# Kernel tuning notes

Measured on AMD Instinct MI355X. Metric: run time of the kernel, lower is better.

The kernel has to match this reference:

```python
import jax, jax.numpy as jnp
import numpy as np
from math import factorial, pi

LMAX = 6      # max angular momentum
NMAX = 5      # max radial index
RC = 3.0      # PolyCut cutoff radius
UNIT = RC / 3.0

_one = np.ones((LMAX + 1, LMAX + 1), np.float32)
YR = jnp.asarray(2.0 * np.tril(_one) - np.eye(LMAX + 1, dtype=np.float32))
YI = jnp.asarray(2.0 * np.triu(_one, k=1))


def _nlm(l, m):
    return float(np.sqrt((2 * l + 1) / (4 * pi) * factorial(l - m) / factorial(l + m)))


def ylm_mat(v):
    """Solid harmonics r^l Y_lm for one point v=(x,y,z).
    Layout (as in AutoForce sph_repr): Re Y_l^m at [l, l-m]; Im Y_l^m at [l-m, l] for m>0,
    so YR (2*tril-eye) weights real parts (m=0 on the diagonal, weight 1) and
    YI (2*triu(1)) weights imaginary parts, reproducing the m-sum of the power spectrum."""
    x, y, z = v[0], v[1], v[2]
    r2 = x * x + y * y + z * z
    # (x + i y)^m by recursion
    A = [jnp.ones((), v.dtype)]
    B = [jnp.zeros((), v.dtype)]
    for m in range(1, LMAX + 1):
        A.append(x * A[m - 1] - y * B[m - 1])
        B.append(x * B[m - 1] + y * A[m - 1])
    # Pi_l^m(z, r^2): homogeneous associated-Legendre part of degree l-m
    Pi = {(0, 0): jnp.ones((), v.dtype)}
    for m in range(1, LMAX + 1):
        Pi[(m, m)] = (2 * m - 1) * Pi[(m - 1, m - 1)]  # (2m-1)!!
    for m in range(0, LMAX):
        Pi[(m + 1, m)] = (2 * m + 1) * z * Pi[(m, m)]
        for l in range(m + 2, LMAX + 1):
            Pi[(l, m)] = ((2 * l - 1) * z * Pi[(l - 1, m)]
                          - (l + m - 1) * r2 * Pi[(l - 2, m)]) / (l - m)
    Y = jnp.zeros((LMAX + 1, LMAX + 1), v.dtype)
    for l in range(LMAX + 1):
        for m in range(l + 1):
            cnl = _nlm(l, m)
            Y = Y.at[l, l - m].set(cnl * Pi[(l, m)] * A[m])
            if m > 0:
                Y = Y.at[l - m, l].set(cnl * Pi[(l, m)] * B[m])
    return Y


def radial(dist):
    # PolyCut: (1 - d/rc)^2 inside rc, and its derivative
    step = (dist < RC).astype(dist.dtype)
    t = 1.0 - dist / RC
    return step * t * t, -2.0 * step * t / RC


def setup_inputs() -> dict:
    key = jax.random.key(0)
    coo = jax.random.normal(key, (150000, 3), dtype=jnp.float32)
    return {"coo": coo}


def reference(coo):
    xyz = coo / UNIT                                   # (N, 3)
    d = jnp.sqrt(jnp.sum(xyz * xyz, axis=-1))          # (N,)
    n = 2.0 * jnp.arange(NMAX + 1, dtype=coo.dtype)    # even powers 0,2,...,2*nmax
    r, dr = radial(UNIT * d)
    dr = UNIT * dr
    f = r[None] * d[None] ** n[:, None]                # (nmax+1, N)
    Y = jnp.transpose(jax.vmap(ylm_mat)(xyz), (1, 2, 0))                   # (L+1, L+1, N)
    dY = jnp.transpose(jax.vmap(jax.jacfwd(ylm_mat))(xyz), (1, 2, 0, 3))   # (L+1, L+1, N, 3)
    c = jnp.einsum('nj,lmj->nlm', f, Y)                # (nmax+1, L+1, L+1)
    # p[i,k,l] = sum_m YR[l,m]*c[i,l,m]*c[k,l,m] + sum_m YI[m,l]*c[i,m,l]*c[k,m,l]
    p = (jnp.einsum('ilm,klm,lm->ikl', c, c, YR)
         + jnp.einsum('iml,kml,ml->ikl', c, c, YI))    # (nmax+1, nmax+1, L+1)
    # hand-derived gradient chain, as in the torch module
    df = dr[None] * d[None] ** n[:, None] + r[None] * n[:, None] * d[None] ** (n[:, None] - 1.0)
    dfv = df[..., None] * xyz / d[:, None]             # (nmax+1, N, 3)
    dc = (dfv[:, None, None] * Y[None, ..., None]
          + f[:, None, None, :, None] * dY[None])      # (nmax+1, L+1, L+1, N, 3)
    # dp without materializing dnnp: contract dc with (c*YR) / (c*YI) directly
    cYr = c * YR
    cYi = c * YI
    dp = (jnp.einsum('klm,ilmjx->ikljx', cYr, dc)
          + jnp.einsum('ilm,klmjx->ikljx', cYr, dc)
          + jnp.einsum('kml,imljx->ikljx', cYi, dc)
          + jnp.einsum('iml,kmljx->ikljx', cYi, dc))   # (nmax+1, nmax+1, L+1, N, 3)
    return p, dp / UNIT
```

## Files before the change

kernel.cpp:

```cpp
#include <hip/hip_runtime.h>


#define LMAXV 6
#define NSZ 6
#define RCV 3.0f

constexpr double csqrt_(double x) {
    double y = x > 1.0 ? x : 1.0;
    for (int i = 0; i < 100; ++i) y = 0.5 * (y + x / y);
    return y;
}
constexpr double factd_(int n) { double r = 1.0; for (int i = 2; i <= n; ++i) r *= i; return r; }
constexpr double PI_D = 3.14159265358979323846;
struct CnlT { float v[7][7]; };
constexpr CnlT make_cnl_() {
    CnlT t{};
    for (int l = 0; l <= 6; ++l)
        for (int m = 0; m <= 6; ++m)
            t.v[l][m] = (m <= l)
                ? (float)csqrt_((2.0 * l + 1.0) / (4.0 * PI_D) * factd_(l - m) / factd_(l + m))
                : 0.0f;
    return t;
}
__device__ constexpr CnlT CNL = make_cnl_();
__device__ constexpr float DFACT[7] = {1.f, 1.f, 3.f, 15.f, 105.f, 945.f, 10395.f};
struct IctT { float v[7][7]; };
constexpr IctT make_ict_() {
    IctT t{};
    for (int l = 0; l <= 6; ++l)
        for (int m = 0; m <= 6; ++m)
            t.v[l][m] = (l > m) ? (float)(1.0 / (double)(l - m)) : 1.0f;
    return t;
}
__device__ constexpr IctT ICT = make_ict_();

__global__ void k_zero(float* __restrict__ cws) {
    int t = blockIdx.x * blockDim.x + threadIdx.x;
    if (t < NSZ * 49) cws[t] = 0.0f;
}

__global__ __launch_bounds__(256) void k_creduce(const float* __restrict__ coo,
                                                 float* __restrict__ cws, int N) {
    const int i_rad = blockIdx.y;
    float acc[7][7];
#pragma unroll
    for (int a = 0; a < 7; ++a)
#pragma unroll
        for (int b = 0; b < 7; ++b) acc[a][b] = 0.0f;

    const int stride = gridDim.x * blockDim.x;
    for (int j = blockIdx.x * blockDim.x + threadIdx.x; j < N; j += stride) {
        float x = coo[3 * j + 0], y = coo[3 * j + 1], z = coo[3 * j + 2];
        float r2 = x * x + y * y + z * z;
        float dn = sqrtf(r2);
        float tt = 1.0f - dn * (1.0f / RCV);
        float r  = (dn < RCV) ? tt * tt : 0.0f;
        float fi = r;
        for (int q = 0; q < i_rad; ++q) fi *= r2;

        float Av[7], Bv[7];
        Av[0] = 1.0f; Bv[0] = 0.0f;
#pragma unroll
        for (int m = 1; m <= 6; ++m) {
            Av[m] = x * Av[m - 1] - y * Bv[m - 1];
            Bv[m] = x * Bv[m - 1] + y * Av[m - 1];
        }

        float P1[7], P2[7];
#pragma unroll
        for (int l = 0; l <= 6; ++l) {
            float PC[7];
#pragma unroll
            for (int mm = 0; mm <= l; ++mm) {
                float pv;
                if (mm == l)            pv = DFACT[l];
                else if (mm == l - 1)   pv = (float)(2 * l - 1) * z * P1[mm];
                else {
                    float a = (float)(2 * l - 1), b = (float)(l + mm - 1);
                    pv = (a * z * P1[mm] - b * r2 * P2[mm]) * (1.0f / (float)(l - mm));
                }
                PC[mm] = pv;
                float base = fi * CNL.v[l][mm] * pv;
                acc[l][l - mm] += base * Av[mm];
                if (mm >= 1) acc[l - mm][l] += base * Bv[mm];
            }
#pragma unroll
            for (int mm = 0; mm <= l; ++mm) { P2[mm] = P1[mm]; P1[mm] = PC[mm]; }
        }
    }

    __shared__ float sblk[49];
    if (threadIdx.x < 49) sblk[threadIdx.x] = 0.0f;
    __syncthreads();
    const int lane = threadIdx.x & 63;
#pragma unroll
    for (int a = 0; a < 7; ++a)
#pragma unroll
        for (int b = 0; b < 7; ++b) {
            float v = acc[a][b];
            v += __shfl_down(v, 32);
            v += __shfl_down(v, 16);
            v += __shfl_down(v, 8);
            v += __shfl_down(v, 4);
            v += __shfl_down(v, 2);
            v += __shfl_down(v, 1);
            if (lane == 0) atomicAdd(&sblk[a * 7 + b], v);
        }
    __syncthreads();
    if (threadIdx.x < 49) atomicAdd(&cws[i_rad * 49 + threadIdx.x], sblk[threadIdx.x]);
}

__global__ void k_p(const float* __restrict__ cws, float* __restrict__ out) {
    int t = threadIdx.x;
    if (t >= 252) return;
    int i = t / 42, k = (t / 7) % 6, l = t % 7;
    const float* ci = cws + i * 49;
    const float* ck = cws + k * 49;
    float s = 0.0f;
    for (int mm = 0; mm <= l; ++mm) {
        float w = (mm == 0) ? 1.0f : 2.0f;
        s += w * ci[l * 7 + (l - mm)] * ck[l * 7 + (l - mm)];
        if (mm >= 1) s += 2.0f * ci[(l - mm) * 7 + l] * ck[(l - mm) * 7 + l];
    }
    out[t] = s;
}

__global__ __launch_bounds__(256) void k_dp(const float* __restrict__ coo,
                                            const float* __restrict__ cws,
                                            float* __restrict__ out, int N) {
    __shared__ float sRe[7][7][6];
    __shared__ float sIm[7][7][6];
    for (int s = threadIdx.x; s < 294; s += blockDim.x) {
        int k = s % 6; int lm = s / 6; int l = lm / 7; int mm = lm % 7;
        float re = 0.0f, im = 0.0f;
        if (mm <= l)            re = ((mm == 0) ? 1.0f : 2.0f) * cws[k * 49 + l * 7 + (l - mm)];
        if (mm >= 1 && mm <= l) im = 2.0f * cws[k * 49 + (l - mm) * 7 + l];
        sRe[l][mm][k] = re;
        sIm[l][mm][k] = im;
    }
    __syncthreads();

    const int j = blockIdx.x * blockDim.x + threadIdx.x;
    if (j >= N) return;

    const float x = coo[3 * j + 0], y = coo[3 * j + 1], z = coo[3 * j + 2];
    const float r2 = x * x + y * y + z * z;
    const float dn = sqrtf(r2);
    const float invd = 1.0f / dn;
    const float tt = 1.0f - dn * (1.0f / RCV);
    const bool  ins = dn < RCV;
    const float r  = ins ? tt * tt : 0.0f;
    const float dr = ins ? (-2.0f / RCV) * tt : 0.0f;

    float f[NSZ], dfx[NSZ], dfy[NSZ], dfz[NSZ];
    {
        const float ux = x * invd, uy = y * invd, uz = z * invd;
        float p2 = 1.0f;
#pragma unroll
        for (int i = 0; i < NSZ; ++i) {
            f[i] = r * p2;
            float dfi = p2 * (dr + (float)(2 * i) * r * invd);
            dfx[i] = dfi * ux; dfy[i] = dfi * uy; dfz[i] = dfi * uz;
            p2 *= r2;
        }
    }

    float Av[7], Ax[7], Ay[7], Bv[7], Bx[7], By[7];
    Av[0] = 1.0f; Ax[0] = 0.0f; Ay[0] = 0.0f;
    Bv[0] = 0.0f; Bx[0] = 0.0f; By[0] = 0.0f;
#pragma unroll
    for (int m = 1; m <= 6; ++m) {
        Av[m] = x * Av[m - 1] - y * Bv[m - 1];
        Ax[m] = Av[m - 1] + x * Ax[m - 1] - y * Bx[m - 1];
        Ay[m] = -Bv[m - 1] + x * Ay[m - 1] - y * By[m - 1];
        Bv[m] = x * Bv[m - 1] + y * Av[m - 1];
        Bx[m] = Bv[m - 1] + x * Bx[m - 1] + y * Ax[m - 1];
        By[m] = Av[m - 1] + x * By[m - 1] + y * Ay[m - 1];
    }

    float P1v[7], P1z[7], P1r[7], P2v[7], P2z[7], P2r[7];
#pragma unroll
    for (int mm = 0; mm < 7; ++mm) {
        P1v[mm] = 0.f; P1z[mm] = 0.f; P1r[mm] = 0.f;
        P2v[mm] = 0.f; P2z[mm] = 0.f; P2r[mm] = 0.f;
    }

    char* const outB = (char*)out;
    const uint32_t lst = (uint32_t)N * 3u;
    uint32_t idxl = 252u + (uint32_t)j * 3u;

#pragma unroll 1
    for (int l = 0; l <= LMAXV; ++l) {
        float S[NSZ], Tx[NSZ], Ty[NSZ], Tz[NSZ];
#pragma unroll
        for (int k = 0; k < NSZ; ++k) { S[k] = 0.0f; Tx[k] = 0.0f; Ty[k] = 0.0f; Tz[k] = 0.0f; }

        const float lf  = (float)l;
        const float a2l = 2.0f * lf - 1.0f;
        const float dfl = DFACT[l];

#pragma unroll
        for (int mm = 0; mm <= 6; ++mm) {
            if (mm <= l) {
                const float b  = lf + (float)(mm - 1);
                const float ic = ICT.v[l][mm];
                float pv = (a2l * z * P1v[mm] - b * r2 * P2v[mm]) * ic;
                float pz = (a2l * (P1v[mm] + z * P1z[mm]) - b * r2 * P2z[mm]) * ic;
                float pr = (a2l * z * P1r[mm] - b * (P2v[mm] + r2 * P2r[mm])) * ic;
                if (mm == l) pv = dfl;
                P2v[mm] = P1v[mm]; P2z[mm] = P1z[mm]; P2r[mm] = P1r[mm];
                P1v[mm] = pv; P1z[mm] = pz; P1r[mm] = pr;

                const float c0  = CNL.v[l][mm];
                const float cp  = c0 * pv;
                const float prx = c0 * 2.0f * pr;
                const float gz  = c0 * pz + prx * z;

                const float ReV = cp * Av[mm];
                const float ReX = prx * x * Av[mm] + cp * Ax[mm];
                const float ReG = prx * y * Av[mm] + cp * Ay[mm];
                const float ReZ = gz * Av[mm];
#pragma unroll
                for (int k = 0; k < NSZ; ++k) {
                    const float cc = sRe[l][mm][k];
                    S[k]  += cc * ReV;
                    Tx[k] += cc * ReX;
                    Ty[k] += cc * ReG;
                    Tz[k] += cc * ReZ;
                }
                if (mm >= 1) {
                    const float ImV = cp * Bv[mm];
                    const float ImX = prx * x * Bv[mm] + cp * Bx[mm];
                    const float ImG = prx * y * Bv[mm] + cp * By[mm];
                    const float ImZ = gz * Bv[mm];
#pragma unroll
                    for (int k = 0; k < NSZ; ++k) {
                        const float cc = sIm[l][mm][k];
                        S[k]  += cc * ImV;
                        Tx[k] += cc * ImX;
                        Ty[k] += cc * ImG;
                        Tz[k] += cc * ImZ;
                    }
                }
            }
        }

#pragma unroll
        for (int i = 0; i < NSZ; ++i)
#pragma unroll
            for (int k = i; k < NSZ; ++k) {
                const float ox = dfx[i] * S[k] + f[i] * Tx[k] + dfx[k] * S[i] + f[k] * Tx[i];
                const float oy = dfy[i] * S[k] + f[i] * Ty[k] + dfy[k] * S[i] + f[k] * Ty[i];
                const float oz = dfz[i] * S[k] + f[i] * Tz[k] + dfz[k] * S[i] + f[k] * Tz[i];
                {
                    const uint32_t b1 = (idxl + (uint32_t)((i * 6 + k) * 7) * lst) * 4u;
                    float* p1 = (float*)(outB + b1);
                    p1[0] = ox; p1[1] = oy; p1[2] = oz;
                }
                if (i != k) {
                    const uint32_t b2 = (idxl + (uint32_t)((k * 6 + i) * 7) * lst) * 4u;
                    float* p2 = (float*)(outB + b2);
                    p2[0] = ox; p2[1] = oy; p2[2] = oz;
                }
            }
        idxl += lst;
    }
}

extern "C" void kernel_launch(void* const* d_in, const int* in_sizes, int n_in,
                              void* d_out, int out_size, void* d_ws, size_t ws_size,
                              hipStream_t stream) {
    const float* coo = (const float*)d_in[0];
    float* out = (float*)d_out;
    float* cws = (float*)d_ws;
    const int N = in_sizes[0] / 3;

    hipLaunchKernelGGL(k_zero, dim3(1), dim3(320), 0, stream, cws);
    hipLaunchKernelGGL(k_creduce, dim3(128, 6), dim3(256), 0, stream, coo, cws, N);
    hipLaunchKernelGGL(k_p, dim3(1), dim3(256), 0, stream, cws, out);
    const int nb = (N + 255) / 256;
    hipLaunchKernelGGL(k_dp, dim3(nb), dim3(256), 0, stream, coo, cws, out, N);
}
```

Baseline: 156.3 us.

## Stage dp outputs through LDS for coalesced 16-byte stores, remap blocks per XCD

Instead of each thread writing three scattered floats per (i,k,l) output directly to global memory, each block stages 12 output slices in shared memory and then writes them out as contiguous float4 stores. All 36 (i,k) pairs are computed explicitly instead of storing symmetric pairs twice. Block indices are also remapped so that each XCD handles a contiguous range of chunks, which is meant to improve L2 locality. The cost is about 36KB of extra LDS, which reduces occupancy, plus two barriers per group of 12 slices. The byte-offset arithmetic assumes the dp region starts 16-byte aligned at offset 1008.

New measurement: 144.9 us. 1.08x faster.

```diff
diff --git a/kernel.cpp b/kernel.cpp
--- a/kernel.cpp
+++ b/kernel.cpp
@@ -4,6 +4,14 @@
 #define LMAXV 6
 #define NSZ 6
 #define RCV 3.0f
+
+typedef float float4v __attribute__((ext_vector_type(4)));
+
+__device__ __forceinline__ void barrier_lds() {
+    asm volatile("s_waitcnt lgkmcnt(0)" ::: "memory");
+    __builtin_amdgcn_sched_barrier(0);
+    __builtin_amdgcn_s_barrier();
+}
 
 constexpr double csqrt_(double x) {
     double y = x > 1.0 ? x : 1.0;
@@ -127,9 +135,12 @@
 
 __global__ __launch_bounds__(256) void k_dp(const float* __restrict__ coo,
                                             const float* __restrict__ cws,
-                                            float* __restrict__ out, int N) {
+                                            float* __restrict__ out, int N,
+                                            int nblk) {
     __shared__ float sRe[7][7][6];
     __shared__ float sIm[7][7][6];
+    __shared__ float stage[12][768];
+
     for (int s = threadIdx.x; s < 294; s += blockDim.x) {
         int k = s % 6; int lm = s / 6; int l = lm / 7; int mm = lm % 7;
         float re = 0.0f, im = 0.0f;
@@ -140,10 +151,17 @@
     }
     __syncthreads();
 
-    const int j = blockIdx.x * blockDim.x + threadIdx.x;
-    if (j >= N) return;
-
-    const float x = coo[3 * j + 0], y = coo[3 * j + 1], z = coo[3 * j + 2];
+    int chunk;
+    {
+        const int b = blockIdx.x;
+        const int q = nblk >> 3, rr = nblk & 7;
+        const int xcd = b & 7, idx = b >> 3;
+        chunk = (xcd < rr ? xcd * (q + 1) : rr * (q + 1) + (xcd - rr) * q) + idx;
+    }
+    const int j0 = chunk * 256;
+    const int jj = min(j0 + (int)threadIdx.x, N - 1);
+
+    const float x = coo[3 * jj + 0], y = coo[3 * jj + 1], z = coo[3 * jj + 2];
     const float r2 = x * x + y * y + z * z;
     const float dn = sqrtf(r2);
     const float invd = 1.0f / dn;
@@ -185,9 +203,11 @@
         P2v[mm] = 0.f; P2z[mm] = 0.f; P2r[mm] = 0.f;
     }
 
+    const uint32_t sliceB = (uint32_t)N * 12u;
+    const uint32_t j0b    = (uint32_t)j0 * 12u;
+    const uint32_t remB   = (uint32_t)(min(256, N - j0)) * 12u;
     char* const outB = (char*)out;
-    const uint32_t lst = (uint32_t)N * 3u;
-    uint32_t idxl = 252u + (uint32_t)j * 3u;
+    const int tid3 = (int)threadIdx.x * 3;
 
 #pragma unroll 1
     for (int l = 0; l <= LMAXV; ++l) {
@@ -245,25 +265,38 @@
             }
         }
 
-#pragma unroll
-        for (int i = 0; i < NSZ; ++i)
-#pragma unroll
-            for (int k = i; k < NSZ; ++k) {
-                const float ox = dfx[i] * S[k] + f[i] * Tx[k] + dfx[k] * S[i] + f[k] * Tx[i];
-                const float oy = dfy[i] * S[k] + f[i] * Ty[k] + dfy[k] * S[i] + f[k] * Ty[i];
-                const float oz = dfz[i] * S[k] + f[i] * Tz[k] + dfz[k] * S[i] + f[k] * Tz[i];
-                {
-                    const uint32_t b1 = (idxl + (uint32_t)((i * 6 + k) * 7) * lst) * 4u;
-                    float* p1 = (float*)(outB + b1);
-                    p1[0] = ox; p1[1] = oy; p1[2] = oz;
-                }
-                if (i != k) {
-                    const uint32_t b2 = (idxl + (uint32_t)((k * 6 + i) * 7) * lst) * 4u;
-                    float* p2 = (float*)(outB + b2);
-                    p2[0] = ox; p2[1] = oy; p2[2] = oz;
+        const uint32_t lbase = 1008u + (uint32_t)l * sliceB + j0b;
+        const uint32_t ikstride = 7u * sliceB;
+#pragma unroll
+        for (int g = 0; g < 3; ++g) {
+#pragma unroll
+            for (int sl = 0; sl < 12; ++sl) {
+                const int s = g * 12 + sl;
+                const int i = s / 6, k = s % 6;
+                const int a = (i < k) ? i : k;
+                const int c = (i < k) ? k : i;
+                const float ox = dfx[a] * S[c] + f[a] * Tx[c] + dfx[c] * S[a] + f[c] * Tx[a];
+                const float oy = dfy[a] * S[c] + f[a] * Ty[c] + dfy[c] * S[a] + f[c] * Ty[a];
+                const float oz = dfz[a] * S[c] + f[a] * Tz[c] + dfz[c] * S[a] + f[c] * Tz[a];
+                stage[sl][tid3 + 0] = ox;
+                stage[sl][tid3 + 1] = oy;
+                stage[sl][tid3 + 2] = oz;
+            }
+            barrier_lds();
+#pragma unroll
+            for (int it = 0; it < 9; ++it) {
+                const int slot = it * 256 + (int)threadIdx.x;
+                const int sl   = slot / 192;
+                const int pos  = slot - sl * 192;
+                const uint32_t boff = (uint32_t)pos << 4;
+                if (boff < remB) {
+                    const int s = g * 12 + sl;
+                    float4v v = *(const float4v*)&stage[sl][pos << 2];
+                    *(float4v*)(outB + lbase + (uint32_t)s * ikstride + boff) = v;
                 }
             }
-        idxl += lst;
+            barrier_lds();
+        }
     }
 }
 
@@ -279,5 +312,5 @@
     hipLaunchKernelGGL(k_creduce, dim3(128, 6), dim3(256), 0, stream, coo, cws, N);
     hipLaunchKernelGGL(k_p, dim3(1), dim3(256), 0, stream, cws, out);
     const int nb = (N + 255) / 256;
-    hipLaunchKernelGGL(k_dp, dim3(nb), dim3(256), 0, stream, coo, cws, out, N);
-}
+    hipLaunchKernelGGL(k_dp, dim3(nb), dim3(256), 0, stream, coo, cws, out, N, nb);
+}
```
